# Performance work log

Hardware: AMD Instinct MI355X
Metric: run time of the kernel (lower is better)

## Reference

```python
import jax, jax.numpy as jnp
import numpy as np

B, S, D = 8, 4096, 256
N_SPANS = 1024
MAX_WIDTH = 32  # static max span width (torch version computes it from data)
MASK_FILL = -1e32


def setup_inputs() -> dict:
    key = jax.random.key(0)
    k1, k2, k3 = jax.random.split(key, 3)
    sequence_tensor = jax.random.normal(k1, (B, S, D), dtype=jnp.float32)
    starts = jax.random.randint(k2, (B, N_SPANS), 0, S - MAX_WIDTH)
    widths = jax.random.randint(k3, (B, N_SPANS), 1, MAX_WIDTH + 1)
    ends = starts + widths  # exclusive end, as the module does span_ends - 1
    span_indices = jnp.stack([starts, ends], axis=-1).astype(jnp.int64)
    return {"sequence_tensor": sequence_tensor, "span_indices": span_indices}


def reference(sequence_tensor, span_indices):
    # starts/ends: (B, N, 1); ends made inclusive
    span_starts = span_indices[..., 0:1]
    span_ends = span_indices[..., 1:2] - 1
    span_widths = span_ends - span_starts  # inclusive width - 1

    # (1, 1, W)
    rng = jnp.arange(MAX_WIDTH, dtype=span_indices.dtype).reshape(1, 1, -1)
    raw_idx = span_ends - rng  # (B, N, W), walks backwards from span end
    span_mask = ((rng <= span_widths) & (raw_idx >= 0)).astype(jnp.float32)
    idx = jnp.maximum(raw_idx, 0)  # relu on indices

    b, n, w = idx.shape
    # gather span token embeddings: (B, N, W, D)
    span_embeddings = jnp.take_along_axis(
        sequence_tensor, idx.reshape(b, n * w, 1), axis=1
    ).reshape(b, n, w, sequence_tensor.shape[-1])

    # global_average_logits is all ones -> gathered logits are ones
    logits = jnp.ones((b, n, w), dtype=jnp.float32)
    masked_logits = jnp.where(span_mask > 0, logits, MASK_FILL)
    weights = jax.nn.softmax(masked_logits, axis=-1)  # (B, N, W)

    # weighted sum over span width -> (B, N, D)
    return jnp.einsum("bnw,bnwd->bnd", weights, span_embeddings)
```

## Files before the change

### kernel.cpp

```cpp
#include <hip/hip_runtime.h>
#include <hip/hip_fp16.h>


constexpr int B = 8;
constexpr int S = 4096;
constexpr int D = 256;
constexpr int N_SPANS = 1024;
constexpr int BLK = 32;
constexpr int NBLK = S / BLK;
constexpr int NWG = B * NBLK;
constexpr int LIST_CAP = 128;

__device__ __forceinline__ float4 f4add(float4 a, float4 b) {
    a.x += b.x; a.y += b.y; a.z += b.z; a.w += b.w; return a;
}

__global__ __launch_bounds__(256) void fused_span_avg_kernel(
    const float* __restrict__ seq,
    const int*   __restrict__ idx32,
    float*       __restrict__ out)
{
    const int gid  = blockIdx.x;
    const int b    = gid & (B - 1);
    const int blk  = gid >> 3;
    const int tid  = threadIdx.x;
    const int wv   = tid >> 6;
    const int lane = tid & 63;

    __shared__ uint2  Pfx[2][BLK][64];
    __shared__ float4 totals[4][64];
    __shared__ unsigned list[LIST_CAP];
    __shared__ int count;

    if (tid == 0) count = 0;
    __syncthreads();

    int row0 = blk * BLK + wv * 16;
    if (row0 > S - 16) row0 = S - 16;
    const float4* src = reinterpret_cast<const float4*>(
        seq + ((size_t)b * S + row0) * D) + lane;
    float4 p[16];
    #pragma unroll
    for (int j = 0; j < 16; ++j) p[j] = src[(size_t)j * (D / 4)];

    const bool is64 = (idx32[1] == 0);
    #pragma unroll
    for (int k = 0; k < 4; ++k) {
        const int n = tid + k * 256;
        int start, end;
        if (is64) {
            const int4 wds = *((const int4*)idx32 + ((size_t)b * N_SPANS + n));
            start = wds.x; end = wds.z;
        } else {
            const int2 wds = *((const int2*)idx32 + ((size_t)b * N_SPANS + n));
            start = wds.x; end = wds.y;
        }
        if ((start >> 5) == blk) {
            const int w     = end - start;
            const int ja    = start & 31;
            const int e     = end - 1;
            const int cross = ((e >> 5) != blk) ? 1 : 0;
            const int jb    = e & 31;
            const unsigned pk = (unsigned)n | ((unsigned)ja << 10) |
                                ((unsigned)jb << 15) | ((unsigned)cross << 20) |
                                ((unsigned)(w - 1) << 21);
            const int slot = atomicAdd(&count, 1);
            if (slot < LIST_CAP) list[slot] = pk;
        }
    }

    #pragma unroll
    for (int j = 1; j < 16; ++j) p[j] = f4add(p[j], p[j - 1]);
    totals[wv][lane] = p[15];
    __syncthreads();

    const int sel = wv >> 1;
    float4 off = make_float4(0.f, 0.f, 0.f, 0.f);
    if (wv & 1) off = totals[wv - 1][lane];

    #pragma unroll
    for (int j = 0; j < 16; ++j) {
        const float4 s = f4add(p[j], off);
        union { __half2 h[2]; uint2 u; } pk2;
        pk2.h[0] = __floats2half2_rn(s.x, s.y);
        pk2.h[1] = __floats2half2_rn(s.z, s.w);
        Pfx[sel][(wv & 1) * 16 + j][lane] = pk2.u;
    }
    __syncthreads();

    auto rd = [&](int selr, int j) -> float4 {
        union { uint2 u; __half2 h[2]; } pk2;
        pk2.u = Pfx[selr][j][lane];
        const float2 a = __half22float2(pk2.h[0]);
        const float2 c = __half22float2(pk2.h[1]);
        return make_float4(a.x, a.y, c.x, c.y);
    };

    const int cnt = (count < LIST_CAP) ? count : LIST_CAP;
    for (int i = wv; i < cnt; i += 4) {
        const unsigned e = list[i];
        const int n     = e & 1023;
        const int ja    = (e >> 10) & 31;
        const int jb    = (e >> 15) & 31;
        const int cross = (e >> 20) & 1;
        const int w     = (int)((e >> 21) & 31) + 1;

        float4 s = rd(cross, jb);
        if (cross) s = f4add(s, rd(0, BLK - 1));
        if (ja) {
            const float4 t = rd(0, ja - 1);
            s.x -= t.x; s.y -= t.y; s.z -= t.z; s.w -= t.w;
        }
        const float inv = 1.0f / (float)w;
        s.x *= inv; s.y *= inv; s.z *= inv; s.w *= inv;
        *((float4*)(out + ((size_t)b * N_SPANS + n) * D) + lane) = s;
    }
}

extern "C" void kernel_launch(void* const* d_in, const int* in_sizes, int n_in,
                              void* d_out, int out_size, void* d_ws, size_t ws_size,
                              hipStream_t stream) {
    const float* seq = (const float*)d_in[0];
    const int*   idx = (const int*)d_in[1];
    float*       out = (float*)d_out;

    fused_span_avg_kernel<<<NWG, 256, 0, stream>>>(seq, idx, out);
}
```

Measured before the change: 13.83 us.

## Serve 96-row chunks per workgroup with four 32-row prefix sub-blocks

Each 512-thread workgroup now loads 128 rows as four independent 32-row prefix-sum sub-blocks and serves every span starting in a 96-row window. This replaces the earlier 32-row blocks that read an extra 32 rows of halo. Halo re-reading drops from 2x to about 1.33x, and the number of index scans and workgroups falls from 1024 to 344. In exchange each workgroup holds more shared memory and there are fewer workgroups to spread across the CUs. Spans that cross into the next sub-block are handled by adding that sub-block's last prefix.

```diff
diff --git a/kernel.cpp b/kernel.cpp
--- a/kernel.cpp
+++ b/kernel.cpp
@@ -6,36 +6,38 @@
 constexpr int S = 4096;
 constexpr int D = 256;
 constexpr int N_SPANS = 1024;
-constexpr int BLK = 32;
-constexpr int NBLK = S / BLK;
-constexpr int NWG = B * NBLK;
-constexpr int LIST_CAP = 128;
+constexpr int SUB = 32;
+constexpr int SERVE = 96;
+constexpr int NCHUNK = 43;
+constexpr int NWG = B * NCHUNK;
+constexpr int LIST_CAP = 192;
 
 __device__ __forceinline__ float4 f4add(float4 a, float4 b) {
     a.x += b.x; a.y += b.y; a.z += b.z; a.w += b.w; return a;
 }
 
-__global__ __launch_bounds__(256) void fused_span_avg_kernel(
+__global__ __launch_bounds__(512, 4) void fused_span_avg_kernel(
     const float* __restrict__ seq,
     const int*   __restrict__ idx32,
     float*       __restrict__ out)
 {
     const int gid  = blockIdx.x;
     const int b    = gid & (B - 1);
-    const int blk  = gid >> 3;
+    const int c    = gid >> 3;
     const int tid  = threadIdx.x;
     const int wv   = tid >> 6;
     const int lane = tid & 63;
 
-    __shared__ uint2  Pfx[2][BLK][64];
-    __shared__ float4 totals[4][64];
+    __shared__ uint2  Pfx[4][SUB][64];
+    __shared__ float4 totals[8][64];
     __shared__ unsigned list[LIST_CAP];
     __shared__ int count;
 
     if (tid == 0) count = 0;
     __syncthreads();
 
-    int row0 = blk * BLK + wv * 16;
+    const int base_start = c * SERVE;
+    int row0 = base_start + wv * 16;
     if (row0 > S - 16) row0 = S - 16;
     const float4* src = reinterpret_cast<const float4*>(
         seq + ((size_t)b * S + row0) * D) + lane;
@@ -45,8 +47,8 @@
 
     const bool is64 = (idx32[1] == 0);
     #pragma unroll
-    for (int k = 0; k < 4; ++k) {
-        const int n = tid + k * 256;
+    for (int k = 0; k < 2; ++k) {
+        const int n = tid + k * 512;
         int start, end;
         if (is64) {
             const int4 wds = *((const int4*)idx32 + ((size_t)b * N_SPANS + n));
@@ -55,15 +57,12 @@
             const int2 wds = *((const int2*)idx32 + ((size_t)b * N_SPANS + n));
             start = wds.x; end = wds.y;
         }
-        if ((start >> 5) == blk) {
-            const int w     = end - start;
-            const int ja    = start & 31;
-            const int e     = end - 1;
-            const int cross = ((e >> 5) != blk) ? 1 : 0;
-            const int jb    = e & 31;
-            const unsigned pk = (unsigned)n | ((unsigned)ja << 10) |
-                                ((unsigned)jb << 15) | ((unsigned)cross << 20) |
-                                ((unsigned)(w - 1) << 21);
+        const int rs = start - base_start;
+        if ((unsigned)rs < (unsigned)SERVE) {
+            const int w  = end - start;
+            const int jb = rs + w - 1;
+            const unsigned pk = (unsigned)n | ((unsigned)rs << 10) |
+                                ((unsigned)jb << 17) | ((unsigned)(w - 1) << 24);
             const int slot = atomicAdd(&count, 1);
             if (slot < LIST_CAP) list[slot] = pk;
         }
@@ -74,9 +73,9 @@
     totals[wv][lane] = p[15];
     __syncthreads();
 
-    const int sel = wv >> 1;
     float4 off = make_float4(0.f, 0.f, 0.f, 0.f);
     if (wv & 1) off = totals[wv - 1][lane];
+    const int sub = wv >> 1;
 
     #pragma unroll
     for (int j = 0; j < 16; ++j) {
@@ -84,31 +83,32 @@
         union { __half2 h[2]; uint2 u; } pk2;
         pk2.h[0] = __floats2half2_rn(s.x, s.y);
         pk2.h[1] = __floats2half2_rn(s.z, s.w);
-        Pfx[sel][(wv & 1) * 16 + j][lane] = pk2.u;
+        Pfx[sub][(wv & 1) * 16 + j][lane] = pk2.u;
     }
     __syncthreads();
 
-    auto rd = [&](int selr, int j) -> float4 {
+    auto rd = [&](int s_, int j) -> float4 {
         union { uint2 u; __half2 h[2]; } pk2;
-        pk2.u = Pfx[selr][j][lane];
+        pk2.u = Pfx[s_][j][lane];
         const float2 a = __half22float2(pk2.h[0]);
-        const float2 c = __half22float2(pk2.h[1]);
-        return make_float4(a.x, a.y, c.x, c.y);
+        const float2 cc = __half22float2(pk2.h[1]);
+        return make_float4(a.x, a.y, cc.x, cc.y);
     };
 
     const int cnt = (count < LIST_CAP) ? count : LIST_CAP;
-    for (int i = wv; i < cnt; i += 4) {
+    for (int i = wv; i < cnt; i += 8) {
         const unsigned e = list[i];
-        const int n     = e & 1023;
-        const int ja    = (e >> 10) & 31;
-        const int jb    = (e >> 15) & 31;
-        const int cross = (e >> 20) & 1;
-        const int w     = (int)((e >> 21) & 31) + 1;
+        const int n  = e & 1023;
+        const int ja = (e >> 10) & 127;
+        const int jb = (e >> 17) & 127;
+        const int w  = (int)((e >> 24) & 31) + 1;
+        const int subA = ja >> 5, ia = ja & 31;
+        const int subB = jb >> 5, ib = jb & 31;
 
-        float4 s = rd(cross, jb);
-        if (cross) s = f4add(s, rd(0, BLK - 1));
-        if (ja) {
-            const float4 t = rd(0, ja - 1);
+        float4 s = rd(subB, ib);
+        if (subB > subA) s = f4add(s, rd(subA, SUB - 1));
+        if (ia) {
+            const float4 t = rd(subA, ia - 1);
             s.x -= t.x; s.y -= t.y; s.z -= t.z; s.w -= t.w;
         }
         const float inv = 1.0f / (float)w;
@@ -124,5 +124,5 @@
     const int*   idx = (const int*)d_in[1];
     float*       out = (float*)d_out;
 
-    fused_span_avg_kernel<<<NWG, 256, 0, stream>>>(seq, idx, out);
+    fused_span_avg_kernel<<<NWG, 512, 0, stream>>>(seq, idx, out);
 }
```

After: 13.20 us. 1.05x faster.
